# Performance work log

Hardware: AMD Instinct MI355X
Metric: run time of the kernel (lower is better)

The kernel has to match this reference:

```python
import jax, jax.numpy as jnp
import numpy as np

NEG_SLOPE = 0.01  # torch F.leaky_relu default used in the DGL GAT-style layer


def grat_layer(h, src, dst, W, a, n_nodes):
    """One GRAT (GAT-style) layer.
    h: [N, d_in], src/dst: [E] int, W: [d_in, d_out], a: [2*d_out] (attn_fc weight
    on concat [z_src || z_dst]). Returns [N, d_out].
    """
    d_out = W.shape[1]
    z = h @ W                                   # [N, d_out]
    # attention logits per edge: a^T [z_src || z_dst]
    s_src = z @ a[:d_out]                       # [N]
    s_dst = z @ a[d_out:]                       # [N]
    e = jax.nn.leaky_relu(s_src[src] + s_dst[dst], NEG_SLOPE)  # [E]
    # numerically stable softmax over incoming edges of each dst node
    m = jax.ops.segment_max(e, dst, num_segments=n_nodes)      # [N]
    m = jnp.where(jnp.isfinite(m), m, 0.0)      # nodes with no in-edges
    w = jnp.exp(e - m[dst])                     # [E]
    denom = jax.ops.segment_sum(w, dst, num_segments=n_nodes)  # [N]
    alpha = w / jnp.maximum(denom, 1e-9)[dst]   # [E]
    # weighted scatter-aggregate of source features into dst
    out = jax.ops.segment_sum(alpha[:, None] * z[src], dst, num_segments=n_nodes)
    return out                                  # [N, d_out]


def setup_inputs() -> dict:
    key = jax.random.key(0)
    ks = jax.random.split(key, 10)
    N, E = 100000, 1600000
    IN, H1, H2, OUT = 128, 32, 32, 1
    feature = jax.random.normal(ks[0], (N, IN), dtype=jnp.float32)
    src = jax.random.randint(ks[1], (E,), 0, N, dtype=jnp.int32)
    dst = jax.random.randint(ks[2], (E,), 0, N, dtype=jnp.int32)
    s = 0.1
    W1 = jax.random.normal(ks[3], (IN, H1), dtype=jnp.float32) * s
    a1 = jax.random.normal(ks[4], (2 * H1,), dtype=jnp.float32) * s
    W2 = jax.random.normal(ks[5], (H1, H2), dtype=jnp.float32) * s
    a2 = jax.random.normal(ks[6], (2 * H2,), dtype=jnp.float32) * s
    W3 = jax.random.normal(ks[7], (H2, OUT), dtype=jnp.float32) * s
    a3 = jax.random.normal(ks[8], (2 * OUT,), dtype=jnp.float32) * s
    return {"feature": feature, "src": src, "dst": dst,
            "W1": W1, "a1": a1, "W2": W2, "a2": a2, "W3": W3, "a3": a3}


def reference(feature, src, dst, W1, a1, W2, a2, W3, a3):
    n = feature.shape[0]
    h = jax.nn.relu(grat_layer(feature, src, dst, W1, a1, n))
    h = jax.nn.relu(grat_layer(h, src, dst, W2, a2, n))
    h = grat_layer(h, src, dst, W3, a3, n)
    return jax.nn.sigmoid(h)                    # [N, 1]
```

## Files before the change

kernel.cpp:

```cpp
#include <hip/hip_runtime.h>
#include <hip/hip_bf16.h>
#include <cstdint>
#include <cstddef>

#define NEG_SLOPE 0.01f

static __device__ __forceinline__ unsigned short f2bf(float f) {
    __hip_bfloat16 b = __float2bfloat16(f);
    return *(unsigned short*)&b;
}


__global__ __launch_bounds__(128) void gemm1_kernel(
    const float* __restrict__ h, const float* __restrict__ W,
    const float* __restrict__ a, unsigned short* __restrict__ zb,
    float* __restrict__ s_src, float* __restrict__ s_dst, int N)
{
    __shared__ float Wl[128 * 32];
    int tid = threadIdx.x;
    int rowBase = blockIdx.x * 64;

    {
        const float4* W4 = (const float4*)W;
        float4* Wl4 = (float4*)Wl;
        for (int i = tid; i < 1024; i += 128) Wl4[i] = W4[i];
    }
    __syncthreads();

    int wv   = tid >> 6;
    int lane = tid & 63;
    int g    = lane >> 3;
    int l8   = lane & 7;
    int r0   = wv * 32 + g * 4;
    int col4 = l8 * 4;

    float acc[4][4];
#pragma unroll
    for (int i = 0; i < 4; i++)
#pragma unroll
        for (int c = 0; c < 4; c++) acc[i][c] = 0.f;

    const float4* h4  = (const float4*)h;
    const float4* Wl4 = (const float4*)Wl;

    size_t rowOff[4];
#pragma unroll
    for (int i = 0; i < 4; i++) {
        int r = rowBase + r0 + i;
        rowOff[i] = (size_t)((r < N) ? r : (N - 1)) * 32;
    }

#pragma unroll 2
    for (int kq = 0; kq < 32; kq++) {
        float4 w0 = Wl4[(kq * 4 + 0) * 8 + l8];
        float4 w1 = Wl4[(kq * 4 + 1) * 8 + l8];
        float4 w2 = Wl4[(kq * 4 + 2) * 8 + l8];
        float4 w3 = Wl4[(kq * 4 + 3) * 8 + l8];
#pragma unroll
        for (int i = 0; i < 4; i++) {
            float4 hv = h4[rowOff[i] + kq];
            acc[i][0] += hv.x * w0.x; acc[i][1] += hv.x * w0.y;
            acc[i][2] += hv.x * w0.z; acc[i][3] += hv.x * w0.w;
            acc[i][0] += hv.y * w1.x; acc[i][1] += hv.y * w1.y;
            acc[i][2] += hv.y * w1.z; acc[i][3] += hv.y * w1.w;
            acc[i][0] += hv.z * w2.x; acc[i][1] += hv.z * w2.y;
            acc[i][2] += hv.z * w2.z; acc[i][3] += hv.z * w2.w;
            acc[i][0] += hv.w * w3.x; acc[i][1] += hv.w * w3.y;
            acc[i][2] += hv.w * w3.z; acc[i][3] += hv.w * w3.w;
        }
    }

    float4 alo = ((const float4*)a)[l8];
    float4 ahi = ((const float4*)a)[8 + l8];
#pragma unroll
    for (int i = 0; i < 4; i++) {
        int row = rowBase + r0 + i;
        if (row < N) {
            ushort4 zv4 = make_ushort4(f2bf(acc[i][0]), f2bf(acc[i][1]),
                                       f2bf(acc[i][2]), f2bf(acc[i][3]));
            *(ushort4*)&zb[(size_t)row * 32 + col4] = zv4;
            float ps = acc[i][0] * alo.x + acc[i][1] * alo.y + acc[i][2] * alo.z + acc[i][3] * alo.w;
            float pd = acc[i][0] * ahi.x + acc[i][1] * ahi.y + acc[i][2] * ahi.z + acc[i][3] * ahi.w;
            ps += __shfl_xor(ps, 1, 64); ps += __shfl_xor(ps, 2, 64); ps += __shfl_xor(ps, 4, 64);
            pd += __shfl_xor(pd, 1, 64); pd += __shfl_xor(pd, 2, 64); pd += __shfl_xor(pd, 4, 64);
            if (l8 == 0) { s_src[row] = ps; s_dst[row] = pd; }
        }
    }
}


#define TILE_E 4096
#define NB_MAX 512

__global__ __launch_bounds__(256) void csr_hist_kernel(
    const int* __restrict__ dst, int* __restrict__ counts,
    int E, int TB, int NB)
{
    __shared__ int hist[NB_MAX];
    int tid = threadIdx.x;
    int t = blockIdx.x;
    for (int b = tid; b < NB; b += 256) hist[b] = 0;
    __syncthreads();
    int base = t * TILE_E;
    for (int i = tid; i < TILE_E; i += 256) {
        int k = base + i;
        if (k < E) atomicAdd(&hist[dst[k] >> 8], 1);
    }
    __syncthreads();
    for (int b = tid; b < NB; b += 256) counts[b * TB + t] = hist[b];
}

__global__ __launch_bounds__(256) void scan1_kernel(
    const int* __restrict__ vals, int* __restrict__ incl,
    int* __restrict__ blockSums, int M)
{
    __shared__ int tmp[256];
    int tid = threadIdx.x;
    int i = blockIdx.x * 256 + tid;
    int v = (i < M) ? vals[i] : 0;
    tmp[tid] = v;
    __syncthreads();
#pragma unroll
    for (int off = 1; off < 256; off <<= 1) {
        int t = (tid >= off) ? tmp[tid - off] : 0;
        __syncthreads();
        tmp[tid] += t;
        __syncthreads();
    }
    if (i < M) incl[i] = tmp[tid];
    if (tid == 255) blockSums[blockIdx.x] = tmp[255];
}

__global__ __launch_bounds__(256) void scan3_kernel(
    const int* __restrict__ vals, const int* __restrict__ blockSums,
    int* __restrict__ cscan, int M, int E)
{
    __shared__ int red[256];
    int tid = threadIdx.x;
    int bid = blockIdx.x;
    int partial = 0;
    for (int j = tid; j < bid; j += 256) partial += blockSums[j];
    red[tid] = partial;
    __syncthreads();
#pragma unroll
    for (int off = 128; off > 0; off >>= 1) {
        if (tid < off) red[tid] += red[tid + off];
        __syncthreads();
    }
    int prefix = red[0];
    int i = bid * 256 + tid;
    if (i < M) cscan[i] = cscan[i] - vals[i] + prefix;
    if (i == 0) cscan[M] = E;
}

__global__ __launch_bounds__(256) void csr_scatter_kernel(
    const int* __restrict__ src, const int* __restrict__ dst,
    const int* __restrict__ cscan, int* __restrict__ ebuf,
    int E, int TB, int NB)
{
    __shared__ int baseB[NB_MAX];
    __shared__ int cur[NB_MAX];
    int tid = threadIdx.x;
    int t = blockIdx.x;
    for (int b = tid; b < NB; b += 256) {
        baseB[b] = cscan[b * TB + t];
        cur[b] = 0;
    }
    __syncthreads();
    int base = t * TILE_E;
    for (int i = tid; i < TILE_E; i += 256) {
        int k = base + i;
        if (k < E) {
            int d = dst[k], s = src[k];
            int b = d >> 8;
            int r = atomicAdd(&cur[b], 1);
            ebuf[baseB[b] + r] = (s << 8) | (d & 255);
        }
    }
}

__global__ __launch_bounds__(256) void csr_bucket_kernel(
    const int* __restrict__ ebuf, const int* __restrict__ cscan,
    int* __restrict__ csr_src, int* __restrict__ offsets,
    int N, int E, int TB)
{
    __shared__ int eb[8192];
    __shared__ int hist[256];
    __shared__ int loff[256];
    __shared__ int tmp[256];
    int tid = threadIdx.x;
    int b = blockIdx.x;

    int beg = cscan[b * TB];
    int endv = cscan[(b + 1) * TB];
    int cnt = endv - beg;
    int first = b << 8;

    hist[tid] = 0;
    __syncthreads();

    bool inLds = (cnt <= 8192);
    for (int i = tid; i < cnt; i += 256) {
        int v = ebuf[beg + i];
        if (inLds) eb[i] = v;
        atomicAdd(&hist[v & 255], 1);
    }
    __syncthreads();

    int hv = hist[tid];
    tmp[tid] = hv;
    __syncthreads();
#pragma unroll
    for (int off = 1; off < 256; off <<= 1) {
        int t = (tid >= off) ? tmp[tid - off] : 0;
        __syncthreads();
        tmp[tid] += t;
        __syncthreads();
    }
    loff[tid] = tmp[tid] - hv;
    __syncthreads();

    if (first + tid < N) offsets[first + tid] = beg + loff[tid];
    if (b == 0 && tid == 0) offsets[N] = E;

    hist[tid] = 0;
    __syncthreads();

    for (int i = tid; i < cnt; i += 256) {
        int v = inLds ? eb[i] : ebuf[beg + i];
        int d8 = v & 255;
        int r = atomicAdd(&hist[d8], 1);
        csr_src[beg + loff[d8] + r] = v >> 8;
    }
}


struct NodePre {
    int beg, end, deg, s_pre;
    float sd, w_pre;
};

__device__ __forceinline__ NodePre agg_preload(
    int node, int N, int lane,
    const int* __restrict__ offsets, const int* __restrict__ csr_src,
    const float* __restrict__ s_src, const float* __restrict__ s_dst)
{
    NodePre r;
    int nodeC = (node < N) ? node : (N - 1);
    r.beg = offsets[nodeC];
    r.end = offsets[nodeC + 1];
    r.deg = r.end - r.beg;
    r.sd  = s_dst[nodeC];
    int pfx = r.beg + lane;
    bool fast = (r.deg <= 32) && (pfx < r.end);
    r.s_pre = fast ? csr_src[pfx] : 0;
    r.w_pre = 0.f;
    if (fast) {
        float e = s_src[r.s_pre] + r.sd;
        e = (e > 0.f) ? e : NEG_SLOPE * e;
        r.w_pre = __expf(e);
    }
    return r;
}

__device__ __forceinline__ float4 agg_core(
    int lane, NodePre np,
    const int* __restrict__ csr_src,
    const float* __restrict__ s_src,
    const unsigned short* __restrict__ zb)
{
    int q = lane >> 3;
    unsigned cb = (unsigned)(lane & 7) * 8u;
    const char* zbc = (const char*)zb;
    float4 o4 = make_float4(0.f, 0.f, 0.f, 0.f);
    float rden;

    if (np.deg <= 32) {
        int soff = np.s_pre << 6;
        int e0 = __shfl(soff, q + 0,  32);
        int e1 = __shfl(soff, q + 4,  32);
        int e2 = __shfl(soff, q + 8,  32);
        int e3 = __shfl(soff, q + 12, 32);
        uint2 g0 = *(const uint2*)(zbc + (cb + (unsigned)e0));
        uint2 g1 = *(const uint2*)(zbc + (cb + (unsigned)e1));
        uint2 g2 = *(const uint2*)(zbc + (cb + (unsigned)e2));
        uint2 g3 = *(const uint2*)(zbc + (cb + (unsigned)e3));
        int dgt = (np.deg > 16);
        uint2 g4, g5, g6, g7;
        if (dgt) {
            int e4 = __shfl(soff, q + 16, 32);
            int e5 = __shfl(soff, q + 20, 32);
            int e6 = __shfl(soff, q + 24, 32);
            int e7 = __shfl(soff, q + 28, 32);
            g4 = *(const uint2*)(zbc + (cb + (unsigned)e4));
            g5 = *(const uint2*)(zbc + (cb + (unsigned)e5));
            g6 = *(const uint2*)(zbc + (cb + (unsigned)e6));
            g7 = *(const uint2*)(zbc + (cb + (unsigned)e7));
        }
        float l = np.w_pre;
#pragma unroll
        for (int off = 16; off > 0; off >>= 1) l += __shfl_xor(l, off, 32);
        rden = 1.f / fmaxf(l, 1e-9f);
        float w0 = __shfl(np.w_pre, q + 0,  32);
        float w1 = __shfl(np.w_pre, q + 4,  32);
        float w2 = __shfl(np.w_pre, q + 8,  32);
        float w3 = __shfl(np.w_pre, q + 12, 32);
        o4.x += w0 * __uint_as_float(g0.x << 16);
        o4.y += w0 * __uint_as_float(g0.x & 0xffff0000u);
        o4.z += w0 * __uint_as_float(g0.y << 16);
        o4.w += w0 * __uint_as_float(g0.y & 0xffff0000u);
        o4.x += w1 * __uint_as_float(g1.x << 16);
        o4.y += w1 * __uint_as_float(g1.x & 0xffff0000u);
        o4.z += w1 * __uint_as_float(g1.y << 16);
        o4.w += w1 * __uint_as_float(g1.y & 0xffff0000u);
        o4.x += w2 * __uint_as_float(g2.x << 16);
        o4.y += w2 * __uint_as_float(g2.x & 0xffff0000u);
        o4.z += w2 * __uint_as_float(g2.y << 16);
        o4.w += w2 * __uint_as_float(g2.y & 0xffff0000u);
        o4.x += w3 * __uint_as_float(g3.x << 16);
        o4.y += w3 * __uint_as_float(g3.x & 0xffff0000u);
        o4.z += w3 * __uint_as_float(g3.y << 16);
        o4.w += w3 * __uint_as_float(g3.y & 0xffff0000u);
        if (dgt) {
            float w4 = __shfl(np.w_pre, q + 16, 32);
            float w5 = __shfl(np.w_pre, q + 20, 32);
            float w6 = __shfl(np.w_pre, q + 24, 32);
            float w7 = __shfl(np.w_pre, q + 28, 32);
            o4.x += w4 * __uint_as_float(g4.x << 16);
            o4.y += w4 * __uint_as_float(g4.x & 0xffff0000u);
            o4.z += w4 * __uint_as_float(g4.y << 16);
            o4.w += w4 * __uint_as_float(g4.y & 0xffff0000u);
            o4.x += w5 * __uint_as_float(g5.x << 16);
            o4.y += w5 * __uint_as_float(g5.x & 0xffff0000u);
            o4.z += w5 * __uint_as_float(g5.y << 16);
            o4.w += w5 * __uint_as_float(g5.y & 0xffff0000u);
            o4.x += w6 * __uint_as_float(g6.x << 16);
            o4.y += w6 * __uint_as_float(g6.x & 0xffff0000u);
            o4.z += w6 * __uint_as_float(g6.y << 16);
            o4.w += w6 * __uint_as_float(g6.y & 0xffff0000u);
            o4.x += w7 * __uint_as_float(g7.x << 16);
            o4.y += w7 * __uint_as_float(g7.x & 0xffff0000u);
            o4.z += w7 * __uint_as_float(g7.y << 16);
            o4.w += w7 * __uint_as_float(g7.y & 0xffff0000u);
        }
    } else {
        float l = 0.f;
        for (int p = np.beg + lane; p < np.end; p += 32) {
            float e = s_src[csr_src[p]] + np.sd;
            e = (e > 0.f) ? e : NEG_SLOPE * e;
            l += __expf(e);
        }
#pragma unroll
        for (int off = 16; off > 0; off >>= 1) l += __shfl_xor(l, off, 32);
        rden = 1.f / fmaxf(l, 1e-9f);
        for (int p = 0; p < np.deg; p += 4) {
            int idx = p + q;
            int valid = (idx < np.deg);
            int s = csr_src[np.beg + (valid ? idx : np.deg - 1)];
            float e = s_src[s] + np.sd;
            e = (e > 0.f) ? e : NEG_SLOPE * e;
            float w = valid ? __expf(e) : 0.f;
            uint2 u = *(const uint2*)(zbc + (cb + ((unsigned)s << 6)));
            o4.x += w * __uint_as_float(u.x << 16);
            o4.y += w * __uint_as_float(u.x & 0xffff0000u);
            o4.z += w * __uint_as_float(u.y << 16);
            o4.w += w * __uint_as_float(u.y & 0xffff0000u);
        }
    }

    o4.x += __shfl_xor(o4.x, 8, 32);
    o4.y += __shfl_xor(o4.y, 8, 32);
    o4.z += __shfl_xor(o4.z, 8, 32);
    o4.w += __shfl_xor(o4.w, 8, 32);
    o4.x += __shfl_xor(o4.x, 16, 32);
    o4.y += __shfl_xor(o4.y, 16, 32);
    o4.z += __shfl_xor(o4.z, 16, 32);
    o4.w += __shfl_xor(o4.w, 16, 32);
    float4 vv4;
    vv4.x = fmaxf(o4.x * rden, 0.f);
    vv4.y = fmaxf(o4.y * rden, 0.f);
    vv4.z = fmaxf(o4.z * rden, 0.f);
    vv4.w = fmaxf(o4.w * rden, 0.f);
    return vv4;
}

__global__ __launch_bounds__(256) void agg32_l1_kernel(
    const int* __restrict__ offsets, const int* __restrict__ csr_src,
    const float* __restrict__ s_src1, const float* __restrict__ s_dst1,
    const unsigned short* __restrict__ zb1,
    const float* __restrict__ W2, const float* __restrict__ a2,
    unsigned short* __restrict__ zb2,
    float* __restrict__ s_src2, float* __restrict__ s_dst2, int N)
{
    __shared__ float W2l[32 * 32];
    __shared__ float hl[16 * 32];
    int tid  = threadIdx.x;
    int g    = tid >> 5;
    int lane = tid & 31;
    int nodeA = blockIdx.x * 16 + g;
    int nodeB = nodeA + 8;

    NodePre pA = agg_preload(nodeA, N, lane, offsets, csr_src, s_src1, s_dst1);
    NodePre pB = agg_preload(nodeB, N, lane, offsets, csr_src, s_src1, s_dst1);

    for (int i = tid; i < 1024; i += 256) W2l[i] = W2[i];
    __syncthreads();

    int c4 = (lane & 7) * 4;
    float a2lo = a2[lane];
    float a2hi = a2[32 + lane];

    {
        float4 vv4 = agg_core(lane, pA, csr_src, s_src1, zb1);
        if ((lane >> 3) == 0) *(float4*)&hl[g * 32 + c4] = vv4;
        const float4* hb4 = (const float4*)&hl[g * 32];
        float acc2 = 0.f;
#pragma unroll
        for (int c = 0; c < 8; ++c) {
            float4 hv = hb4[c];
            acc2 += hv.x * W2l[(c * 4 + 0) * 32 + lane];
            acc2 += hv.y * W2l[(c * 4 + 1) * 32 + lane];
            acc2 += hv.z * W2l[(c * 4 + 2) * 32 + lane];
            acc2 += hv.w * W2l[(c * 4 + 3) * 32 + lane];
        }
        float ps = acc2 * a2lo;
        float pd = acc2 * a2hi;
#pragma unroll
        for (int off = 16; off > 0; off >>= 1) {
            ps += __shfl_xor(ps, off, 32);
            pd += __shfl_xor(pd, off, 32);
        }
        if (nodeA < N) {
            zb2[(size_t)nodeA * 32 + lane] = f2bf(acc2);
            if (lane == 0) { s_src2[nodeA] = ps; s_dst2[nodeA] = pd; }
        }
    }

    {
        float4 vv4 = agg_core(lane, pB, csr_src, s_src1, zb1);
        if ((lane >> 3) == 0) *(float4*)&hl[(8 + g) * 32 + c4] = vv4;
        const float4* hb4 = (const float4*)&hl[(8 + g) * 32];
        float acc2 = 0.f;
#pragma unroll
        for (int c = 0; c < 8; ++c) {
            float4 hv = hb4[c];
            acc2 += hv.x * W2l[(c * 4 + 0) * 32 + lane];
            acc2 += hv.y * W2l[(c * 4 + 1) * 32 + lane];
            acc2 += hv.z * W2l[(c * 4 + 2) * 32 + lane];
            acc2 += hv.w * W2l[(c * 4 + 3) * 32 + lane];
        }
        float ps = acc2 * a2lo;
        float pd = acc2 * a2hi;
#pragma unroll
        for (int off = 16; off > 0; off >>= 1) {
            ps += __shfl_xor(ps, off, 32);
            pd += __shfl_xor(pd, off, 32);
        }
        if (nodeB < N) {
            zb2[(size_t)nodeB * 32 + lane] = f2bf(acc2);
            if (lane == 0) { s_src2[nodeB] = ps; s_dst2[nodeB] = pd; }
        }
    }
}

__global__ __launch_bounds__(256) void agg32_l2_kernel(
    const int* __restrict__ offsets, const int* __restrict__ csr_src,
    const float* __restrict__ s_src2, const float* __restrict__ s_dst2,
    const unsigned short* __restrict__ zb2,
    const float* __restrict__ W3, const float* __restrict__ a3,
    float* __restrict__ zs, float* __restrict__ s_dst3, int N)
{
    int tid  = threadIdx.x;
    int g    = tid >> 5;
    int lane = tid & 31;
    int nodeA = blockIdx.x * 16 + g;
    int nodeB = nodeA + 8;

    NodePre pA = agg_preload(nodeA, N, lane, offsets, csr_src, s_src2, s_dst2);
    NodePre pB = agg_preload(nodeB, N, lane, offsets, csr_src, s_src2, s_dst2);

    float4 w3q = ((const float4*)W3)[lane & 7];
    float a31 = a3[1];

    {
        float4 vv4 = agg_core(lane, pA, csr_src, s_src2, zb2);
        float t = vv4.x * w3q.x + vv4.y * w3q.y + vv4.z * w3q.z + vv4.w * w3q.w;
        t += __shfl_xor(t, 1, 32);
        t += __shfl_xor(t, 2, 32);
        t += __shfl_xor(t, 4, 32);
        if (nodeA < N && lane == 0) {
            zs[nodeA] = t;
            s_dst3[nodeA] = t * a31;
        }
    }
    {
        float4 vv4 = agg_core(lane, pB, csr_src, s_src2, zb2);
        float t = vv4.x * w3q.x + vv4.y * w3q.y + vv4.z * w3q.z + vv4.w * w3q.w;
        t += __shfl_xor(t, 1, 32);
        t += __shfl_xor(t, 2, 32);
        t += __shfl_xor(t, 4, 32);
        if (nodeB < N && lane == 0) {
            zs[nodeB] = t;
            s_dst3[nodeB] = t * a31;
        }
    }
}

__global__ __launch_bounds__(256) void agg1_fused_kernel(
    const int* __restrict__ offsets, const int* __restrict__ csr_src,
    const float* __restrict__ zs, const float* __restrict__ a3,
    const float* __restrict__ s_dst, float* __restrict__ out, int N)
{
    int node = blockIdx.x * 8 + (threadIdx.x >> 5);
    int lane = threadIdx.x & 31;
    if (node >= N) return;

    int beg = offsets[node], end = offsets[node + 1];
    float sd = s_dst[node];
    float a30 = a3[0];

    float l = 0.f, o = 0.f;
    for (int p = beg + lane; p < end; p += 32) {
        float z = zs[csr_src[p]];
        float e = z * a30 + sd;
        e = (e > 0.f) ? e : NEG_SLOPE * e;
        float w = __expf(e);
        l += w;
        o += w * z;
    }
#pragma unroll
    for (int off = 16; off > 0; off >>= 1) {
        l += __shfl_xor(l, off, 32);
        o += __shfl_xor(o, off, 32);
    }
    if (lane == 0) {
        float v = o / fmaxf(l, 1e-9f);
        out[node] = 1.f / (1.f + __expf(-v));
    }
}


extern "C" void kernel_launch(void* const* d_in, const int* in_sizes, int n_in,
                              void* d_out, int out_size, void* d_ws, size_t ws_size,
                              hipStream_t stream)
{
    const float* feature = (const float*)d_in[0];
    const int*   src     = (const int*)d_in[1];
    const int*   dst     = (const int*)d_in[2];
    const float* W1      = (const float*)d_in[3];
    const float* a1      = (const float*)d_in[4];
    const float* W2      = (const float*)d_in[5];
    const float* a2      = (const float*)d_in[6];
    const float* W3      = (const float*)d_in[7];
    const float* a3      = (const float*)d_in[8];
    float* out = (float*)d_out;

    const int N = in_sizes[0] / 128;
    const int E = in_sizes[1];

    const int TB = (E + TILE_E - 1) / TILE_E;
    const int NB = (N + 255) >> 8;
    const int M  = NB * TB;

    char* p = (char*)d_ws;
    unsigned short* zb1 = (unsigned short*)p;  p += (size_t)N * 32 * sizeof(unsigned short);
    unsigned short* zb2 = (unsigned short*)p;  p += (size_t)N * 32 * sizeof(unsigned short);
    float* zs32    = (float*)p;  p += (size_t)N * 2 * sizeof(float);
    float* s_src1  = (float*)p;  p += (size_t)N * sizeof(float);
    float* s_dst1  = (float*)p;  p += (size_t)N * sizeof(float);
    float* s_src2  = (float*)p;  p += (size_t)N * sizeof(float);
    float* s_dst2  = (float*)p;  p += (size_t)N * sizeof(float);
    float* s_dst3  = (float*)p;  p += (size_t)N * sizeof(float);
    int*   offsets = (int*)p;    p += ((size_t)N + 1) * sizeof(int);
    int*   counts  = (int*)p;    p += ((size_t)M + 1) * sizeof(int);
    int*   cscan   = (int*)p;    p += ((size_t)M + 1) * sizeof(int);
    int*   blockSums = (int*)p;  p += 1024 * sizeof(int);
    int*   ebuf    = (int*)p;    p += (size_t)E * sizeof(int);
    int*   csr_src = (int*)p;    p += (size_t)E * sizeof(int);

    const int nodeBlocks8  = (N + 7) / 8;
    const int nodeBlocks16 = (N + 15) / 16;
    const int gemmBlocks64 = (N + 63) / 64;
    const int scanBlocksM  = (M + 255) / 256;

    hipLaunchKernelGGL(csr_hist_kernel, dim3(TB), dim3(256), 0, stream,
                       dst, counts, E, TB, NB);
    hipLaunchKernelGGL(scan1_kernel, dim3(scanBlocksM), dim3(256), 0, stream,
                       counts, cscan, blockSums, M);
    hipLaunchKernelGGL(scan3_kernel, dim3(scanBlocksM), dim3(256), 0, stream,
                       counts, blockSums, cscan, M, E);
    hipLaunchKernelGGL(csr_scatter_kernel, dim3(TB), dim3(256), 0, stream,
                       src, dst, cscan, ebuf, E, TB, NB);
    hipLaunchKernelGGL(csr_bucket_kernel, dim3(NB), dim3(256), 0, stream,
                       ebuf, cscan, csr_src, offsets, N, E, TB);

    hipLaunchKernelGGL(gemm1_kernel, dim3(gemmBlocks64), dim3(128), 0, stream,
                       feature, W1, a1, zb1, s_src1, s_dst1, N);
    hipLaunchKernelGGL(agg32_l1_kernel, dim3(nodeBlocks16), dim3(256), 0, stream,
                       offsets, csr_src, s_src1, s_dst1, zb1, W2, a2,
                       zb2, s_src2, s_dst2, N);

    hipLaunchKernelGGL(agg32_l2_kernel, dim3(nodeBlocks16), dim3(256), 0, stream,
                       offsets, csr_src, s_src2, s_dst2, zb2, W3, a3,
                       zs32, s_dst3, N);

    hipLaunchKernelGGL(agg1_fused_kernel, dim3(nodeBlocks8), dim3(256), 0, stream,
                       offsets, csr_src, zs32, a3, s_dst3, out, N);
}
```

Before: 240.9 us.

## Issue both nodes' feature gathers before consuming, and halve CSR edge tile size

Splits the aggregation core into an issue phase that launches the bf16 feature gathers for both nodes a warp handles, and a consume phase that does the weighted accumulation. The softmax denominator reduction moves into the preload. This puts the two nodes' gather latency in flight together instead of one after another, and moves the high-degree path into its own non-inlined function. It also halves the CSR build edge tile to make more blocks, and enlarges the blockSums buffer to fit the larger count array. The cost is higher register pressure from holding two gather buffers, which may lower occupancy.

```diff
diff --git a/kernel.cpp b/kernel.cpp
--- a/kernel.cpp
+++ b/kernel.cpp
@@ -89,7 +89,7 @@
 }
 
 
-#define TILE_E 4096
+#define TILE_E 2048
 #define NB_MAX 512
 
 __global__ __launch_bounds__(256) void csr_hist_kernel(
@@ -237,7 +237,12 @@
 
 struct NodePre {
     int beg, end, deg, s_pre;
-    float sd, w_pre;
+    float sd, w_pre, rden;
+};
+
+struct GBuf {
+    uint2 g0, g1, g2, g3, g4, g5, g6, g7;
+    int dgt;
 };
 
 __device__ __forceinline__ NodePre agg_preload(
@@ -260,114 +265,45 @@
         e = (e > 0.f) ? e : NEG_SLOPE * e;
         r.w_pre = __expf(e);
     }
+    float l = r.w_pre;
+#pragma unroll
+    for (int off = 16; off > 0; off >>= 1) l += __shfl_xor(l, off, 32);
+    r.rden = 1.f / fmaxf(l, 1e-9f);
     return r;
 }
 
-__device__ __forceinline__ float4 agg_core(
-    int lane, NodePre np,
-    const int* __restrict__ csr_src,
-    const float* __restrict__ s_src,
-    const unsigned short* __restrict__ zb)
-{
+__device__ __forceinline__ GBuf agg_issue(
+    int lane, const NodePre& np, const unsigned short* __restrict__ zb)
+{
+    GBuf G;
     int q = lane >> 3;
     unsigned cb = (unsigned)(lane & 7) * 8u;
     const char* zbc = (const char*)zb;
-    float4 o4 = make_float4(0.f, 0.f, 0.f, 0.f);
-    float rden;
-
-    if (np.deg <= 32) {
-        int soff = np.s_pre << 6;
-        int e0 = __shfl(soff, q + 0,  32);
-        int e1 = __shfl(soff, q + 4,  32);
-        int e2 = __shfl(soff, q + 8,  32);
-        int e3 = __shfl(soff, q + 12, 32);
-        uint2 g0 = *(const uint2*)(zbc + (cb + (unsigned)e0));
-        uint2 g1 = *(const uint2*)(zbc + (cb + (unsigned)e1));
-        uint2 g2 = *(const uint2*)(zbc + (cb + (unsigned)e2));
-        uint2 g3 = *(const uint2*)(zbc + (cb + (unsigned)e3));
-        int dgt = (np.deg > 16);
-        uint2 g4, g5, g6, g7;
-        if (dgt) {
-            int e4 = __shfl(soff, q + 16, 32);
-            int e5 = __shfl(soff, q + 20, 32);
-            int e6 = __shfl(soff, q + 24, 32);
-            int e7 = __shfl(soff, q + 28, 32);
-            g4 = *(const uint2*)(zbc + (cb + (unsigned)e4));
-            g5 = *(const uint2*)(zbc + (cb + (unsigned)e5));
-            g6 = *(const uint2*)(zbc + (cb + (unsigned)e6));
-            g7 = *(const uint2*)(zbc + (cb + (unsigned)e7));
-        }
-        float l = np.w_pre;
-#pragma unroll
-        for (int off = 16; off > 0; off >>= 1) l += __shfl_xor(l, off, 32);
-        rden = 1.f / fmaxf(l, 1e-9f);
-        float w0 = __shfl(np.w_pre, q + 0,  32);
-        float w1 = __shfl(np.w_pre, q + 4,  32);
-        float w2 = __shfl(np.w_pre, q + 8,  32);
-        float w3 = __shfl(np.w_pre, q + 12, 32);
-        o4.x += w0 * __uint_as_float(g0.x << 16);
-        o4.y += w0 * __uint_as_float(g0.x & 0xffff0000u);
-        o4.z += w0 * __uint_as_float(g0.y << 16);
-        o4.w += w0 * __uint_as_float(g0.y & 0xffff0000u);
-        o4.x += w1 * __uint_as_float(g1.x << 16);
-        o4.y += w1 * __uint_as_float(g1.x & 0xffff0000u);
-        o4.z += w1 * __uint_as_float(g1.y << 16);
-        o4.w += w1 * __uint_as_float(g1.y & 0xffff0000u);
-        o4.x += w2 * __uint_as_float(g2.x << 16);
-        o4.y += w2 * __uint_as_float(g2.x & 0xffff0000u);
-        o4.z += w2 * __uint_as_float(g2.y << 16);
-        o4.w += w2 * __uint_as_float(g2.y & 0xffff0000u);
-        o4.x += w3 * __uint_as_float(g3.x << 16);
-        o4.y += w3 * __uint_as_float(g3.x & 0xffff0000u);
-        o4.z += w3 * __uint_as_float(g3.y << 16);
-        o4.w += w3 * __uint_as_float(g3.y & 0xffff0000u);
-        if (dgt) {
-            float w4 = __shfl(np.w_pre, q + 16, 32);
-            float w5 = __shfl(np.w_pre, q + 20, 32);
-            float w6 = __shfl(np.w_pre, q + 24, 32);
-            float w7 = __shfl(np.w_pre, q + 28, 32);
-            o4.x += w4 * __uint_as_float(g4.x << 16);
-            o4.y += w4 * __uint_as_float(g4.x & 0xffff0000u);
-            o4.z += w4 * __uint_as_float(g4.y << 16);
-            o4.w += w4 * __uint_as_float(g4.y & 0xffff0000u);
-            o4.x += w5 * __uint_as_float(g5.x << 16);
-            o4.y += w5 * __uint_as_float(g5.x & 0xffff0000u);
-            o4.z += w5 * __uint_as_float(g5.y << 16);
-            o4.w += w5 * __uint_as_float(g5.y & 0xffff0000u);
-            o4.x += w6 * __uint_as_float(g6.x << 16);
-            o4.y += w6 * __uint_as_float(g6.x & 0xffff0000u);
-            o4.z += w6 * __uint_as_float(g6.y << 16);
-            o4.w += w6 * __uint_as_float(g6.y & 0xffff0000u);
-            o4.x += w7 * __uint_as_float(g7.x << 16);
-            o4.y += w7 * __uint_as_float(g7.x & 0xffff0000u);
-            o4.z += w7 * __uint_as_float(g7.y << 16);
-            o4.w += w7 * __uint_as_float(g7.y & 0xffff0000u);
-        }
-    } else {
-        float l = 0.f;
-        for (int p = np.beg + lane; p < np.end; p += 32) {
-            float e = s_src[csr_src[p]] + np.sd;
-            e = (e > 0.f) ? e : NEG_SLOPE * e;
-            l += __expf(e);
-        }
-#pragma unroll
-        for (int off = 16; off > 0; off >>= 1) l += __shfl_xor(l, off, 32);
-        rden = 1.f / fmaxf(l, 1e-9f);
-        for (int p = 0; p < np.deg; p += 4) {
-            int idx = p + q;
-            int valid = (idx < np.deg);
-            int s = csr_src[np.beg + (valid ? idx : np.deg - 1)];
-            float e = s_src[s] + np.sd;
-            e = (e > 0.f) ? e : NEG_SLOPE * e;
-            float w = valid ? __expf(e) : 0.f;
-            uint2 u = *(const uint2*)(zbc + (cb + ((unsigned)s << 6)));
-            o4.x += w * __uint_as_float(u.x << 16);
-            o4.y += w * __uint_as_float(u.x & 0xffff0000u);
-            o4.z += w * __uint_as_float(u.y << 16);
-            o4.w += w * __uint_as_float(u.y & 0xffff0000u);
-        }
-    }
-
+    int soff = np.s_pre << 6;
+    int e0 = __shfl(soff, q + 0,  32);
+    int e1 = __shfl(soff, q + 4,  32);
+    int e2 = __shfl(soff, q + 8,  32);
+    int e3 = __shfl(soff, q + 12, 32);
+    G.g0 = *(const uint2*)(zbc + (cb + (unsigned)e0));
+    G.g1 = *(const uint2*)(zbc + (cb + (unsigned)e1));
+    G.g2 = *(const uint2*)(zbc + (cb + (unsigned)e2));
+    G.g3 = *(const uint2*)(zbc + (cb + (unsigned)e3));
+    G.dgt = (np.deg > 16);
+    if (G.dgt) {
+        int e4 = __shfl(soff, q + 16, 32);
+        int e5 = __shfl(soff, q + 20, 32);
+        int e6 = __shfl(soff, q + 24, 32);
+        int e7 = __shfl(soff, q + 28, 32);
+        G.g4 = *(const uint2*)(zbc + (cb + (unsigned)e4));
+        G.g5 = *(const uint2*)(zbc + (cb + (unsigned)e5));
+        G.g6 = *(const uint2*)(zbc + (cb + (unsigned)e6));
+        G.g7 = *(const uint2*)(zbc + (cb + (unsigned)e7));
+    }
+    return G;
+}
+
+__device__ __forceinline__ float4 agg_finish(float4 o4, float rden)
+{
     o4.x += __shfl_xor(o4.x, 8, 32);
     o4.y += __shfl_xor(o4.y, 8, 32);
     o4.z += __shfl_xor(o4.z, 8, 32);
@@ -384,6 +320,91 @@
     return vv4;
 }
 
+__device__ __forceinline__ float4 agg_consume(
+    int lane, const NodePre& np, const GBuf& G)
+{
+    int q = lane >> 3;
+    float4 o4 = make_float4(0.f, 0.f, 0.f, 0.f);
+    float w0 = __shfl(np.w_pre, q + 0,  32);
+    float w1 = __shfl(np.w_pre, q + 4,  32);
+    float w2 = __shfl(np.w_pre, q + 8,  32);
+    float w3 = __shfl(np.w_pre, q + 12, 32);
+    o4.x += w0 * __uint_as_float(G.g0.x << 16);
+    o4.y += w0 * __uint_as_float(G.g0.x & 0xffff0000u);
+    o4.z += w0 * __uint_as_float(G.g0.y << 16);
+    o4.w += w0 * __uint_as_float(G.g0.y & 0xffff0000u);
+    o4.x += w1 * __uint_as_float(G.g1.x << 16);
+    o4.y += w1 * __uint_as_float(G.g1.x & 0xffff0000u);
+    o4.z += w1 * __uint_as_float(G.g1.y << 16);
+    o4.w += w1 * __uint_as_float(G.g1.y & 0xffff0000u);
+    o4.x += w2 * __uint_as_float(G.g2.x << 16);
+    o4.y += w2 * __uint_as_float(G.g2.x & 0xffff0000u);
+    o4.z += w2 * __uint_as_float(G.g2.y << 16);
+    o4.w += w2 * __uint_as_float(G.g2.y & 0xffff0000u);
+    o4.x += w3 * __uint_as_float(G.g3.x << 16);
+    o4.y += w3 * __uint_as_float(G.g3.x & 0xffff0000u);
+    o4.z += w3 * __uint_as_float(G.g3.y << 16);
+    o4.w += w3 * __uint_as_float(G.g3.y & 0xffff0000u);
+    if (G.dgt) {
+        float w4 = __shfl(np.w_pre, q + 16, 32);
+        float w5 = __shfl(np.w_pre, q + 20, 32);
+        float w6 = __shfl(np.w_pre, q + 24, 32);
+        float w7 = __shfl(np.w_pre, q + 28, 32);
+        o4.x += w4 * __uint_as_float(G.g4.x << 16);
+        o4.y += w4 * __uint_as_float(G.g4.x & 0xffff0000u);
+        o4.z += w4 * __uint_as_float(G.g4.y << 16);
+        o4.w += w4 * __uint_as_float(G.g4.y & 0xffff0000u);
+        o4.x += w5 * __uint_as_float(G.g5.x << 16);
+        o4.y += w5 * __uint_as_float(G.g5.x & 0xffff0000u);
+        o4.z += w5 * __uint_as_float(G.g5.y << 16);
+        o4.w += w5 * __uint_as_float(G.g5.y & 0xffff0000u);
+        o4.x += w6 * __uint_as_float(G.g6.x << 16);
+        o4.y += w6 * __uint_as_float(G.g6.x & 0xffff0000u);
+        o4.z += w6 * __uint_as_float(G.g6.y << 16);
+        o4.w += w6 * __uint_as_float(G.g6.y & 0xffff0000u);
+        o4.x += w7 * __uint_as_float(G.g7.x << 16);
+        o4.y += w7 * __uint_as_float(G.g7.x & 0xffff0000u);
+        o4.z += w7 * __uint_as_float(G.g7.y << 16);
+        o4.w += w7 * __uint_as_float(G.g7.y & 0xffff0000u);
+    }
+    return agg_finish(o4, np.rden);
+}
+
+__device__ float4 agg_slow(
+    int lane, const NodePre& np,
+    const int* __restrict__ csr_src,
+    const float* __restrict__ s_src,
+    const unsigned short* __restrict__ zb)
+{
+    int q = lane >> 3;
+    unsigned cb = (unsigned)(lane & 7) * 8u;
+    const char* zbc = (const char*)zb;
+    float4 o4 = make_float4(0.f, 0.f, 0.f, 0.f);
+    float l = 0.f;
+    for (int p = np.beg + lane; p < np.end; p += 32) {
+        float e = s_src[csr_src[p]] + np.sd;
+        e = (e > 0.f) ? e : NEG_SLOPE * e;
+        l += __expf(e);
+    }
+#pragma unroll
+    for (int off = 16; off > 0; off >>= 1) l += __shfl_xor(l, off, 32);
+    float rden = 1.f / fmaxf(l, 1e-9f);
+    for (int p = 0; p < np.deg; p += 4) {
+        int idx = p + q;
+        int valid = (idx < np.deg);
+        int s = csr_src[np.beg + (valid ? idx : np.deg - 1)];
+        float e = s_src[s] + np.sd;
+        e = (e > 0.f) ? e : NEG_SLOPE * e;
+        float w = valid ? __expf(e) : 0.f;
+        uint2 u = *(const uint2*)(zbc + (cb + ((unsigned)s << 6)));
+        o4.x += w * __uint_as_float(u.x << 16);
+        o4.y += w * __uint_as_float(u.x & 0xffff0000u);
+        o4.z += w * __uint_as_float(u.y << 16);
+        o4.w += w * __uint_as_float(u.y & 0xffff0000u);
+    }
+    return agg_finish(o4, rden);
+}
+
 __global__ __launch_bounds__(256) void agg32_l1_kernel(
     const int* __restrict__ offsets, const int* __restrict__ csr_src,
     const float* __restrict__ s_src1, const float* __restrict__ s_dst1,
@@ -410,8 +431,15 @@
     float a2lo = a2[lane];
     float a2hi = a2[32 + lane];
 
+    bool fastA = (pA.deg <= 32);
+    bool fastB = (pB.deg <= 32);
+    GBuf GA, GB;
+    if (fastA) GA = agg_issue(lane, pA, zb1);
+    if (fastB) GB = agg_issue(lane, pB, zb1);
+
     {
-        float4 vv4 = agg_core(lane, pA, csr_src, s_src1, zb1);
+        float4 vv4 = fastA ? agg_consume(lane, pA, GA)
+                           : agg_slow(lane, pA, csr_src, s_src1, zb1);
         if ((lane >> 3) == 0) *(float4*)&hl[g * 32 + c4] = vv4;
         const float4* hb4 = (const float4*)&hl[g * 32];
         float acc2 = 0.f;
@@ -437,7 +465,8 @@
     }
 
     {
-        float4 vv4 = agg_core(lane, pB, csr_src, s_src1, zb1);
+        float4 vv4 = fastB ? agg_consume(lane, pB, GB)
+                           : agg_slow(lane, pB, csr_src, s_src1, zb1);
         if ((lane >> 3) == 0) *(float4*)&hl[(8 + g) * 32 + c4] = vv4;
         const float4* hb4 = (const float4*)&hl[(8 + g) * 32];
         float acc2 = 0.f;
@@ -482,8 +511,15 @@
     float4 w3q = ((const float4*)W3)[lane & 7];
     float a31 = a3[1];
 
+    bool fastA = (pA.deg <= 32);
+    bool fastB = (pB.deg <= 32);
+    GBuf GA, GB;
+    if (fastA) GA = agg_issue(lane, pA, zb2);
+    if (fastB) GB = agg_issue(lane, pB, zb2);
+
     {
-        float4 vv4 = agg_core(lane, pA, csr_src, s_src2, zb2);
+        float4 vv4 = fastA ? agg_consume(lane, pA, GA)
+                           : agg_slow(lane, pA, csr_src, s_src2, zb2);
         float t = vv4.x * w3q.x + vv4.y * w3q.y + vv4.z * w3q.z + vv4.w * w3q.w;
         t += __shfl_xor(t, 1, 32);
         t += __shfl_xor(t, 2, 32);
@@ -494,7 +530,8 @@
         }
     }
     {
-        float4 vv4 = agg_core(lane, pB, csr_src, s_src2, zb2);
+        float4 vv4 = fastB ? agg_consume(lane, pB, GB)
+                           : agg_slow(lane, pB, csr_src, s_src2, zb2);
         float t = vv4.x * w3q.x + vv4.y * w3q.y + vv4.z * w3q.z + vv4.w * w3q.w;
         t += __shfl_xor(t, 1, 32);
         t += __shfl_xor(t, 2, 32);
@@ -574,7 +611,7 @@
     int*   offsets = (int*)p;    p += ((size_t)N + 1) * sizeof(int);
     int*   counts  = (int*)p;    p += ((size_t)M + 1) * sizeof(int);
     int*   cscan   = (int*)p;    p += ((size_t)M + 1) * sizeof(int);
-    int*   blockSums = (int*)p;  p += 1024 * sizeof(int);
+    int*   blockSums = (int*)p;  p += 4096 * sizeof(int);
     int*   ebuf    = (int*)p;    p += (size_t)E * sizeof(int);
     int*   csr_src = (int*)p;    p += (size_t)E * sizeof(int);
 
```

Result: slower. 248.1 us (+3.0%).
